# Kernel tuning notes

Hardware: AMD Instinct MI355X
Metric: run time of the kernel (lower is better)

The kernel has to match this reference:

```python
import jax, jax.numpy as jnp
import numpy as np

D_MODEL = 1024
N_HEAD = 16


def setup_inputs() -> dict:
    key = jax.random.key(0)
    k1, k2, k3 = jax.random.split(key, 3)
    scale = 1.0 / np.sqrt(D_MODEL)
    x = jax.random.normal(k1, (1, 4096, D_MODEL), dtype=jnp.float32)
    # nn.Linear weights stored as [out, in]; applied as x @ W.T
    w_attn = jax.random.normal(k2, (3 * D_MODEL, D_MODEL), dtype=jnp.float32) * scale
    w_proj = jax.random.normal(k3, (D_MODEL, D_MODEL), dtype=jnp.float32) * scale
    return {"x": x, "w_attn": w_attn, "w_proj": w_proj}


def reference(x, w_attn, w_proj):
    B, T, C = x.shape
    H = N_HEAD
    hd = C // H
    qkv = x @ w_attn.T                      # [B, T, 3C]
    q, k, v = jnp.split(qkv, 3, axis=-1)
    # [B, T, C] -> [B, H, T, hd]
    q = q.reshape(B, T, H, hd).transpose(0, 2, 1, 3)
    k = k.reshape(B, T, H, hd).transpose(0, 2, 1, 3)
    v = v.reshape(B, T, H, hd).transpose(0, 2, 1, 3)
    att = jnp.einsum("bhqd,bhkd->bhqk", q, k) * (1.0 / np.sqrt(hd))  # [B,H,T,T]
    causal = jnp.tril(jnp.ones((T, T), dtype=bool))
    att = jnp.where(causal[None, None], att, -jnp.inf)
    att = jax.nn.softmax(att, axis=-1)
    y = jnp.einsum("bhqk,bhkd->bhqd", att, v)  # [B,H,T,hd]
    y = y.transpose(0, 2, 1, 3).reshape(B, T, C)
    return y @ w_proj.T
```

## Files before the change

### kernel.cpp

```cpp
#include <hip/hip_runtime.h>
#include <hip/hip_bf16.h>
#include <stdint.h>

typedef __bf16 bf16x8 __attribute__((ext_vector_type(8)));
typedef float f32x4 __attribute__((ext_vector_type(4)));

#define T_SEQ 4096
#define C_DIM 1024
#define H_NUM 16
#define HD 64
#define C3 3072
#define NEG_BIG (-30000.0f)

__device__ __forceinline__ unsigned short f2bf(float f) {
    uint32_t u = __builtin_bit_cast(uint32_t, f);
    u += 0x7fffu + ((u >> 16) & 1u);
    return (unsigned short)(u >> 16);
}

__device__ __forceinline__ uint32_t pk_bf16(float a, float b) {
    __hip_bfloat162 h = __float22bfloat162_rn(float2{a, b});
    uint32_t u;
    __builtin_memcpy(&u, &h, sizeof(u));
    return u;
}

__device__ __forceinline__ bf16x8 ld_bf8(const unsigned short* p) {
    return *reinterpret_cast<const bf16x8*>(p);
}

__device__ __forceinline__ void async_g2l16(const unsigned short* g, unsigned short* l) {
    __builtin_amdgcn_global_load_lds(
        (const __attribute__((address_space(1))) void*)g,
        (__attribute__((address_space(3))) void*)l, 16, 0, 0);
}

__device__ __forceinline__ void store_c(unsigned short* C, size_t idx, float v) { C[idx] = f2bf(v); }
__device__ __forceinline__ void store_c(float* C, size_t idx, float v)          { C[idx] = v; }

__device__ __forceinline__ void cvt8(const float* src, unsigned short* dst) {
    float4 f0 = *(const float4*)src;
    float4 f1 = *(const float4*)(src + 4);
    union { uint32_t w[4]; uint4 q; } t;
    t.w[0] = pk_bf16(f0.x, f0.y);
    t.w[1] = pk_bf16(f0.z, f0.w);
    t.w[2] = pk_bf16(f1.x, f1.y);
    t.w[3] = pk_bf16(f1.z, f1.w);
    *(uint4*)dst = t.q;
}

__global__ void cvt_xw(const float* __restrict__ x, const float* __restrict__ wa,
                       unsigned short* __restrict__ xb, unsigned short* __restrict__ wab) {
    int i = (blockIdx.x * blockDim.x + threadIdx.x) * 8;
    if (i < T_SEQ * C_DIM) cvt8(x + i, xb + i);
    else {
        int k = i - T_SEQ * C_DIM;
        if (k < C3 * C_DIM) cvt8(wa + k, wab + k);
    }
}

__global__ void cvt_f32_bf16(const float* __restrict__ src, unsigned short* __restrict__ dst, int n) {
    int i = (blockIdx.x * blockDim.x + threadIdx.x) * 8;
    if (i >= n) return;
    cvt8(src + i, dst + i);
}

__global__ __launch_bounds__(256) void v_transpose(
    const unsigned short* __restrict__ qkv, unsigned short* __restrict__ Vt)
{
    __shared__ unsigned short tile[64][72];
    const int t0 = blockIdx.x * 64, c0 = blockIdx.y * 64;
    const int r = threadIdx.x >> 2, q = threadIdx.x & 3;

    const unsigned short* src = qkv + (size_t)(t0 + r) * C3 + 2 * C_DIM + c0 + q * 16;
    *(uint4*)&tile[r][q * 16]     = *(const uint4*)src;
    *(uint4*)&tile[r][q * 16 + 8] = *(const uint4*)(src + 8);
    __syncthreads();

    union { unsigned short u[16]; uint4 v[2]; } o;
    #pragma unroll
    for (int j = 0; j < 16; ++j) o.u[j] = tile[q * 16 + j][r];
    unsigned short* dst = Vt + (size_t)(c0 + r) * T_SEQ + t0 + q * 16;
    *(uint4*)dst       = o.v[0];
    *(uint4*)(dst + 8) = o.v[1];
}

template <typename TC>
__global__ __launch_bounds__(256, 2) void gemm_bt(
    const unsigned short* __restrict__ A, const unsigned short* __restrict__ B,
    TC* __restrict__ C, int M, int N, int K)
{
    __shared__ __attribute__((aligned(16))) unsigned short As[128 * 32];
    __shared__ __attribute__((aligned(16))) unsigned short Bs[128 * 32];

    const int tid  = threadIdx.x;
    const int wave = tid >> 6, lane = tid & 63;
    const int quad = lane >> 4, l16 = lane & 15;
    const int wm = wave >> 1, wn = wave & 1;
    const int m0 = blockIdx.y * 128, n0 = blockIdx.x * 128;

    const int srow = wave * 32 + (lane >> 2);
    const int scol = (lane & 3) * 8;

    f32x4 acc[4][4] = {};

    for (int k0 = 0; k0 < K; k0 += 32) {
        {
            const unsigned short* ga = A + (size_t)(m0 + srow) * K + k0 + scol;
            const unsigned short* gb = B + (size_t)(n0 + srow) * K + k0 + scol;
            unsigned short* la = As + (wave * 32) * 32;
            unsigned short* lb = Bs + (wave * 32) * 32;
            async_g2l16(ga, la);
            async_g2l16(ga + (size_t)16 * K, la + 16 * 32);
            async_g2l16(gb, lb);
            async_g2l16(gb + (size_t)16 * K, lb + 16 * 32);
        }
        __syncthreads();

        bf16x8 af[4], bf[4];
        #pragma unroll
        for (int i = 0; i < 4; ++i) {
            af[i] = ld_bf8(As + (wm * 64 + i * 16 + l16) * 32 + quad * 8);
            bf[i] = ld_bf8(Bs + (wn * 64 + i * 16 + l16) * 32 + quad * 8);
        }
        #pragma unroll
        for (int mt = 0; mt < 4; ++mt)
            #pragma unroll
            for (int nt = 0; nt < 4; ++nt)
                acc[mt][nt] = __builtin_amdgcn_mfma_f32_16x16x32_bf16(
                    af[mt], bf[nt], acc[mt][nt], 0, 0, 0);
        __syncthreads();
    }

    #pragma unroll
    for (int mt = 0; mt < 4; ++mt)
        #pragma unroll
        for (int nt = 0; nt < 4; ++nt)
            #pragma unroll
            for (int r = 0; r < 4; ++r) {
                int row = m0 + wm * 64 + mt * 16 + quad * 4 + r;
                int col = n0 + wn * 64 + nt * 16 + l16;
                store_c(C, (size_t)row * N + col, acc[mt][nt][r]);
            }
}

template <bool MASK>
__device__ __forceinline__ void fa7_tile(
    const unsigned short* Ksb, const unsigned short* Vsb, unsigned short* pbuf,
    const bf16x8 qf[2][2], f32x4 o[2][4], float* l_part,
    int k0, int q_abs0, int quad, int l16, int sw, int fo0, int fo1)
{
    const unsigned short* krow = Ksb + l16 * 64;
    bf16x8 kf[4][2];
    #pragma unroll
    for (int s = 0; s < 4; ++s) {
        kf[s][0] = ld_bf8(krow + s * 1024 + fo0);
        kf[s][1] = ld_bf8(krow + s * 1024 + fo1);
    }

    #pragma unroll
    for (int qs = 0; qs < 2; ++qs) {
        f32x4 st[4];
        #pragma unroll
        for (int s = 0; s < 4; ++s) {
            f32x4 z = {};
            z = __builtin_amdgcn_mfma_f32_16x16x32_bf16(kf[s][0], qf[qs][0], z, 0, 0, 0);
            st[s] = __builtin_amdgcn_mfma_f32_16x16x32_bf16(kf[s][1], qf[qs][1], z, 0, 0, 0);
        }
        float ts = 0.f;
        #pragma unroll
        for (int s = 0; s < 4; ++s)
            #pragma unroll
            for (int r = 0; r < 4; ++r) {
                float v = st[s][r];
                if (MASK) {
                    int key = k0 + s * 16 + quad * 4 + r;
                    v = (key <= q_abs0 + qs * 16) ? v : NEG_BIG;
                }
                float e = __builtin_amdgcn_exp2f(v);
                st[s][r] = e;
                ts += e;
            }
        l_part[qs] += ts;

        unsigned short* prow = pbuf + (qs * 16 + l16) * 64;
        #pragma unroll
        for (int s = 0; s < 4; ++s) {
            int g = 2 * s + (quad >> 1);
            uint2 pk;
            pk.x = pk_bf16(st[s][0], st[s][1]);
            pk.y = pk_bf16(st[s][2], st[s][3]);
            *(uint2*)((char*)prow + (g ^ sw) * 16 + 8 * (quad & 1)) = pk;
        }
    }

    const unsigned short* vrow = Vsb + l16 * 64;
    bf16x8 vf[4][2];
    #pragma unroll
    for (int c = 0; c < 4; ++c) {
        vf[c][0] = ld_bf8(vrow + c * 1024 + fo0);
        vf[c][1] = ld_bf8(vrow + c * 1024 + fo1);
    }
    #pragma unroll
    for (int qs = 0; qs < 2; ++qs) {
        const unsigned short* prow = pbuf + (qs * 16 + l16) * 64;
        bf16x8 pf0 = ld_bf8(prow + fo0);
        bf16x8 pf1 = ld_bf8(prow + fo1);
        #pragma unroll
        for (int c = 0; c < 4; ++c) {
            o[qs][c] = __builtin_amdgcn_mfma_f32_16x16x32_bf16(vf[c][0], pf0, o[qs][c], 0, 0, 0);
            o[qs][c] = __builtin_amdgcn_mfma_f32_16x16x32_bf16(vf[c][1], pf1, o[qs][c], 0, 0, 0);
        }
    }
}

__global__ __launch_bounds__(128, 2) void flash_attn7(
    const unsigned short* __restrict__ qkv,
    const unsigned short* __restrict__ Vt,
    unsigned short* __restrict__ Y)
{
    __shared__ __attribute__((aligned(16))) unsigned short Ks[2][64 * 64];
    __shared__ __attribute__((aligned(16))) unsigned short Vs[2][64 * 64];
    __shared__ __attribute__((aligned(16))) unsigned short Pl[2][32 * 64];

    const int tid  = threadIdx.x;
    const int wave = tid >> 6, lane = tid & 63;
    const int quad = lane >> 4, l16 = lane & 15;

    const int bi = blockIdx.x;
    const int rr = bi >> 8, ss = bi & 255;
    const int h  = ss & 15;
    const int j  = ss >> 4;
    const int qb = (rr == 0) ? j : (rr == 1) ? 63 - j : (rr == 2) ? 16 + j : 47 - j;

    const int q0w    = qb * 64 + wave * 32;
    const int q_abs0 = q0w + l16;
    const int sw  = l16 & 7;
    const int fo0 = (quad ^ sw) * 8;
    const int fo1 = ((quad + 4) ^ sw) * 8;

    bf16x8 qf[2][2];
    {
        const float QS = 0.125f * 1.44269504f;
        #pragma unroll
        for (int qs = 0; qs < 2; ++qs) {
            const unsigned short* qp =
                qkv + (size_t)(q0w + qs * 16 + l16) * C3 + h * HD + quad * 8;
            bf16x8 a = ld_bf8(qp), b = ld_bf8(qp + 32);
            #pragma unroll
            for (int i = 0; i < 8; ++i) {
                qf[qs][0][i] = (__bf16)((float)a[i] * QS);
                qf[qs][1][i] = (__bf16)((float)b[i] * QS);
            }
        }
    }

    const int srow = lane >> 3;
    const int schunk = (lane & 7) ^ srow;
    const unsigned short* kp =
        qkv + (size_t)(wave * 32 + srow) * C3 + C_DIM + h * HD + schunk * 8;
    const unsigned short* vp =
        Vt + (size_t)(h * HD + wave * 32 + srow) * T_SEQ + schunk * 8;
    unsigned short* lk = Ks[0] + (wave * 32) * 64;
    unsigned short* lv = Vs[0] + (wave * 32) * 64;
    const int lds_db = 64 * 64;
    const size_t kstep = (size_t)8 * C3;
    const size_t vstep = (size_t)8 * T_SEQ;

    auto stage = [&](int b) {
        #pragma unroll
        for (int jj = 0; jj < 4; ++jj) {
            async_g2l16(kp + jj * kstep, lk + b * lds_db + jj * 8 * 64);
            async_g2l16(vp + jj * vstep, lv + b * lds_db + jj * 8 * 64);
        }
    };

    f32x4 o[2][4] = {};
    float l_part[2] = {0.f, 0.f};
    unsigned short* pbuf = Pl[wave];

    const int ntiles = qb + 1;
    stage(0);
    kp += (size_t)64 * C3; vp += 64;

    for (int t = 0; t < ntiles; ++t) {
        __syncthreads();
        const int b = t & 1;
        if (t + 1 < ntiles) {
            stage(1 - b);
            kp += (size_t)64 * C3; vp += 64;
            fa7_tile<false>(Ks[b], Vs[b], pbuf, qf, o, l_part,
                            t * 64, q_abs0, quad, l16, sw, fo0, fo1);
        } else {
            fa7_tile<true>(Ks[b], Vs[b], pbuf, qf, o, l_part,
                           t * 64, q_abs0, quad, l16, sw, fo0, fo1);
        }
    }

    #pragma unroll
    for (int qs = 0; qs < 2; ++qs) {
        float l = l_part[qs];
        l += __shfl_xor(l, 16, 64);
        l += __shfl_xor(l, 32, 64);
        float inv_l = 1.f / l;
        #pragma unroll
        for (int c = 0; c < 4; ++c) {
            union { uint32_t w[2]; uint2 q; } t;
            t.w[0] = pk_bf16(o[qs][c][0] * inv_l, o[qs][c][1] * inv_l);
            t.w[1] = pk_bf16(o[qs][c][2] * inv_l, o[qs][c][3] * inv_l);
            *(uint2*)(Y + (size_t)(q_abs0 + qs * 16) * C_DIM + h * HD + c * 16 + quad * 4) = t.q;
        }
    }
}

extern "C" void kernel_launch(void* const* d_in, const int* in_sizes, int n_in,
                              void* d_out, int out_size, void* d_ws, size_t ws_size,
                              hipStream_t stream) {
    const float* x      = (const float*)d_in[0];
    const float* w_attn = (const float*)d_in[1];
    const float* w_proj = (const float*)d_in[2];
    float* out = (float*)d_out;

    unsigned short* qkv = (unsigned short*)d_ws;
    unsigned short* xb  = qkv + (size_t)T_SEQ * C3;
    unsigned short* y   = xb;
    unsigned short* wpb = qkv;
    unsigned short* Vt  = (unsigned short*)d_out;
    unsigned short* wab = Vt + (size_t)C_DIM * T_SEQ;

    cvt_xw<<<(T_SEQ * C_DIM + C3 * C_DIM) / 8 / 256, 256, 0, stream>>>(x, w_attn, xb, wab);

    gemm_bt<unsigned short>
        <<<dim3(C3 / 128, T_SEQ / 128), 256, 0, stream>>>(xb, wab, qkv, T_SEQ, C3, C_DIM);

    v_transpose<<<dim3(T_SEQ / 64, C_DIM / 64), 256, 0, stream>>>(qkv, Vt);

    flash_attn7<<<dim3(1024), 128, 0, stream>>>(qkv, Vt, y);

    cvt_f32_bf16<<<(C_DIM * C_DIM / 8 + 255) / 256, 256, 0, stream>>>(w_proj, wpb, C_DIM * C_DIM);
    gemm_bt<float>
        <<<dim3(C_DIM / 128, T_SEQ / 128), 256, 0, stream>>>(y, wpb, out, T_SEQ, C_DIM, C_DIM);
}
```

Baseline: 219.0 us.

## Transpose P in registers with permlane swaps instead of LDS round trip

The softmax probability tile P used to be written to a per-wave LDS buffer and read back in the layout the PV MFMA expects. It is now repacked in registers with permlane32/permlane16 swap instructions, with a shuffle-based fallback, so the LDS store/load and the Pl shared buffer are gone. MFMA phases are also wrapped in s_setprio to raise wave priority around matrix work. The permlane mapping has to match the old swizzled layout exactly, and the extra cross-lane ops plus the priority hints may change how instructions are scheduled.

```diff
diff --git a/kernel.cpp b/kernel.cpp
--- a/kernel.cpp
+++ b/kernel.cpp
@@ -144,11 +144,37 @@
             }
 }
 
+#if __has_builtin(__builtin_amdgcn_permlane32_swap) && __has_builtin(__builtin_amdgcn_permlane16_swap)
+#define HAVE_PERMLANE_SWAP 1
+#else
+#define HAVE_PERMLANE_SWAP 0
+#endif
+
+__device__ __forceinline__ void quad_xpose_pair(uint32_t X, uint32_t Y,
+                                                uint32_t& t0, uint32_t& t1) {
+#if HAVE_PERMLANE_SWAP
+    auto S = __builtin_amdgcn_permlane32_swap((int)X, (int)Y, false, false);
+    auto T = __builtin_amdgcn_permlane16_swap((int)S[0], (int)S[1], false, false);
+    t0 = (uint32_t)T[0];
+    t1 = (uint32_t)T[1];
+#else
+    const unsigned l = threadIdx.x & 63;
+    uint32_t Ys = (uint32_t)__shfl_xor((int)Y, 32, 64);
+    uint32_t Xs = (uint32_t)__shfl_xor((int)X, 32, 64);
+    uint32_t S0 = (l < 32) ? X : Ys;
+    uint32_t S1 = (l < 32) ? Xs : Y;
+    uint32_t S0s = (uint32_t)__shfl_xor((int)S0, 16, 64);
+    uint32_t S1s = (uint32_t)__shfl_xor((int)S1, 16, 64);
+    t0 = (l & 16) ? S1s : S0;
+    t1 = (l & 16) ? S1 : S0s;
+#endif
+}
+
 template <bool MASK>
 __device__ __forceinline__ void fa7_tile(
-    const unsigned short* Ksb, const unsigned short* Vsb, unsigned short* pbuf,
+    const unsigned short* Ksb, const unsigned short* Vsb,
     const bf16x8 qf[2][2], f32x4 o[2][4], float* l_part,
-    int k0, int q_abs0, int quad, int l16, int sw, int fo0, int fo1)
+    int k0, int q_abs0, int quad, int l16, int fo0, int fo1)
 {
     const unsigned short* krow = Ksb + l16 * 64;
     bf16x8 kf[4][2];
@@ -158,15 +184,19 @@
         kf[s][1] = ld_bf8(krow + s * 1024 + fo1);
     }
 
+    bf16x8 pf[2][2];
     #pragma unroll
     for (int qs = 0; qs < 2; ++qs) {
         f32x4 st[4];
+        __builtin_amdgcn_s_setprio(1);
         #pragma unroll
         for (int s = 0; s < 4; ++s) {
             f32x4 z = {};
             z = __builtin_amdgcn_mfma_f32_16x16x32_bf16(kf[s][0], qf[qs][0], z, 0, 0, 0);
             st[s] = __builtin_amdgcn_mfma_f32_16x16x32_bf16(kf[s][1], qf[qs][1], z, 0, 0, 0);
         }
+        __builtin_amdgcn_s_setprio(0);
+
         float ts = 0.f;
         #pragma unroll
         for (int s = 0; s < 4; ++s)
@@ -183,15 +213,19 @@
             }
         l_part[qs] += ts;
 
-        unsigned short* prow = pbuf + (qs * 16 + l16) * 64;
+        uint32_t W[4][2];
         #pragma unroll
         for (int s = 0; s < 4; ++s) {
-            int g = 2 * s + (quad >> 1);
-            uint2 pk;
-            pk.x = pk_bf16(st[s][0], st[s][1]);
-            pk.y = pk_bf16(st[s][2], st[s][3]);
-            *(uint2*)((char*)prow + (g ^ sw) * 16 + 8 * (quad & 1)) = pk;
-        }
+            W[s][0] = pk_bf16(st[s][0], st[s][1]);
+            W[s][1] = pk_bf16(st[s][2], st[s][3]);
+        }
+        union { uint32_t w[4]; bf16x8 v; } pA, pB;
+        quad_xpose_pair(W[0][0], W[1][0], pA.w[0], pA.w[2]);
+        quad_xpose_pair(W[0][1], W[1][1], pA.w[1], pA.w[3]);
+        quad_xpose_pair(W[2][0], W[3][0], pB.w[0], pB.w[2]);
+        quad_xpose_pair(W[2][1], W[3][1], pB.w[1], pB.w[3]);
+        pf[qs][0] = pA.v;
+        pf[qs][1] = pB.v;
     }
 
     const unsigned short* vrow = Vsb + l16 * 64;
@@ -201,17 +235,15 @@
         vf[c][0] = ld_bf8(vrow + c * 1024 + fo0);
         vf[c][1] = ld_bf8(vrow + c * 1024 + fo1);
     }
-    #pragma unroll
-    for (int qs = 0; qs < 2; ++qs) {
-        const unsigned short* prow = pbuf + (qs * 16 + l16) * 64;
-        bf16x8 pf0 = ld_bf8(prow + fo0);
-        bf16x8 pf1 = ld_bf8(prow + fo1);
+    __builtin_amdgcn_s_setprio(1);
+    #pragma unroll
+    for (int qs = 0; qs < 2; ++qs)
         #pragma unroll
         for (int c = 0; c < 4; ++c) {
-            o[qs][c] = __builtin_amdgcn_mfma_f32_16x16x32_bf16(vf[c][0], pf0, o[qs][c], 0, 0, 0);
-            o[qs][c] = __builtin_amdgcn_mfma_f32_16x16x32_bf16(vf[c][1], pf1, o[qs][c], 0, 0, 0);
-        }
-    }
+            o[qs][c] = __builtin_amdgcn_mfma_f32_16x16x32_bf16(vf[c][0], pf[qs][0], o[qs][c], 0, 0, 0);
+            o[qs][c] = __builtin_amdgcn_mfma_f32_16x16x32_bf16(vf[c][1], pf[qs][1], o[qs][c], 0, 0, 0);
+        }
+    __builtin_amdgcn_s_setprio(0);
 }
 
 __global__ __launch_bounds__(128, 2) void flash_attn7(
@@ -221,7 +253,6 @@
 {
     __shared__ __attribute__((aligned(16))) unsigned short Ks[2][64 * 64];
     __shared__ __attribute__((aligned(16))) unsigned short Vs[2][64 * 64];
-    __shared__ __attribute__((aligned(16))) unsigned short Pl[2][32 * 64];
 
     const int tid  = threadIdx.x;
     const int wave = tid >> 6, lane = tid & 63;
@@ -277,7 +308,6 @@
 
     f32x4 o[2][4] = {};
     float l_part[2] = {0.f, 0.f};
-    unsigned short* pbuf = Pl[wave];
 
     const int ntiles = qb + 1;
     stage(0);
@@ -289,11 +319,11 @@
         if (t + 1 < ntiles) {
             stage(1 - b);
             kp += (size_t)64 * C3; vp += 64;
-            fa7_tile<false>(Ks[b], Vs[b], pbuf, qf, o, l_part,
-                            t * 64, q_abs0, quad, l16, sw, fo0, fo1);
+            fa7_tile<false>(Ks[b], Vs[b], qf, o, l_part,
+                            t * 64, q_abs0, quad, l16, fo0, fo1);
         } else {
-            fa7_tile<true>(Ks[b], Vs[b], pbuf, qf, o, l_part,
-                           t * 64, q_abs0, quad, l16, sw, fo0, fo1);
+            fa7_tile<true>(Ks[b], Vs[b], qf, o, l_part,
+                           t * 64, q_abs0, quad, l16, fo0, fo1);
         }
     }
 
```

After: 220.8 us. Within noise of the previous version (+0.8%).
